# Performance work log

Measured on AMD Instinct MI355X. Metric: run time of the kernel, lower is better.

Reference implementation:

```python
import jax
import jax.numpy as jnp
import numpy as np

VOCAB = 16384
WIDTH = 256
BETA = 0.25
EPS = 1e-12  # F.normalize eps


def setup_inputs() -> dict:
    key = jax.random.key(0)
    k1, k2, k3 = jax.random.split(key, 3)
    class_tokens = jax.random.normal(k1, (32, 1, WIDTH), dtype=jnp.float32)
    patch_tokens = jax.random.normal(k2, (32, WIDTH, 16, 16), dtype=jnp.float32)
    W = jax.random.normal(k3, (VOCAB, WIDTH), dtype=jnp.float32) * 0.02  # codebook
    return {"class_tokens": class_tokens, "patch_tokens": patch_tokens, "W": W}


def _l2norm(x):
    return x / jnp.maximum(jnp.linalg.norm(x, axis=-1, keepdims=True), EPS)


def reference(class_tokens, patch_tokens, W):
    B, L, C = class_tokens.shape
    _, _, H, Wd = patch_tokens.shape
    # (B,C,H,W) -> (B,HW,C)
    pt = patch_tokens.reshape(B, C, H * Wd).transpose(0, 2, 1)
    NxC = jnp.concatenate([class_tokens, pt], axis=1).reshape(-1, C)  # [N,C]

    # vocab_norm branch: cosine-similarity argmax on detached, normalized vectors
    xn = _l2norm(jax.lax.stop_gradient(NxC))      # [N,C]
    Wn = _l2norm(W)                                # [V,C] (column-normalized W.T)
    sim = xn @ Wn.T                                # [N,V] big matmul
    idx = jnp.argmax(sim, axis=1)                  # [N]

    counts = jnp.zeros((VOCAB,), jnp.float32).at[idx].add(1.0)  # bincount

    fhat_g = W[idx]                                # codebook gather [N,C]
    vq_loss = BETA * jnp.mean((jax.lax.stop_gradient(fhat_g) - NxC) ** 2) \
              + jnp.mean((fhat_g - jax.lax.stop_gradient(NxC)) ** 2)

    # straight-through estimator
    fhat = jax.lax.stop_gradient(fhat_g - NxC) + NxC

    prob = counts / counts.sum()
    vocab_usage = jnp.mean((prob > 0.01 / VOCAB).astype(jnp.float32)) * 100.0

    fhat = fhat.reshape(B, L + H * Wd, C)
    fhat_class = fhat[:, :L, :]
    fhat_patch = fhat[:, L:, :].reshape(B, H, Wd, C).transpose(0, 3, 1, 2)
    return fhat_class, fhat_patch, vq_loss, vocab_usage
```

## Files before the change

kernel.cpp:

```cpp
#include <hip/hip_runtime.h>
#include <stdint.h>

#define VOCAB 16384
#define NB 32
#define NTOK 8224
#define MTILES 65
#define MP 8320
#define NBY 128
#define TILE_BYTES 65536
#define PHASE_BYTES 16384
#define NLOSS 2056
#define MWIN 2.25e-3f
#define TOKCHUNKS 520

typedef _Float16 half8 __attribute__((ext_vector_type(8)));
typedef float f4 __attribute__((ext_vector_type(4)));
typedef __attribute__((address_space(1))) const uint32_t* gas_t;
typedef __attribute__((address_space(3))) uint32_t* las_t;

__device__ __forceinline__ void async16(const void* g, void* l) {
    __builtin_amdgcn_global_load_lds((gas_t)g, (las_t)l, 16, 0, 0);
}

__device__ __forceinline__ unsigned long long key64(float v, int idx) {
    unsigned u = __float_as_uint(v);
    u = (u & 0x80000000u) ? ~u : (u | 0x80000000u);
    return ((unsigned long long)u << 32) | (unsigned)(~idx);
}

__device__ __forceinline__ float keyval(unsigned long long k) {
    unsigned u = (unsigned)(k >> 32);
    u = (u & 0x80000000u) ? (u & 0x7fffffffu) : ~u;
    return __uint_as_float(u);
}

__device__ __forceinline__ void merge2(unsigned long long& k1, unsigned long long& k2,
                                       unsigned long long p1, unsigned long long p2) {
    unsigned long long lo = k1 < p1 ? k1 : p1;
    k1 = k1 > p1 ? k1 : p1;
    unsigned long long m2 = k2 > p2 ? k2 : p2;
    k2 = lo > m2 ? lo : m2;
}

__global__ __launch_bounds__(256) void k_patch(const float* __restrict__ patch, float* __restrict__ tok) {
    __shared__ float t[64][65];
    int c0 = blockIdx.x * 64, p0 = blockIdx.y * 64, b = blockIdx.z;
    int tid = threadIdx.x;
    int l = tid & 63, w = tid >> 6;
    const float* src = patch + b * 65536;
#pragma unroll
    for (int i = 0; i < 16; ++i) {
        int row = i * 4 + w;
        t[row][l] = src[(c0 + row) * 256 + p0 + l];
    }
    __syncthreads();
#pragma unroll
    for (int i = 0; i < 16; ++i) {
        int prow = i * 4 + w;
        tok[(b * 257 + 1 + p0 + prow) * 256 + c0 + l] = t[l][prow];
    }
}

__global__ __launch_bounds__(256) void k_pack2(const float* __restrict__ tok, const float* __restrict__ cls,
                                               const float* __restrict__ W, char* __restrict__ apk,
                                               char* __restrict__ bpk, float* __restrict__ ntokv,
                                               float* __restrict__ nwv) {
    __shared__ float t[16][264];
    __shared__ float pr[16][16];
    __shared__ float sn[16];
    int g0 = blockIdx.x;
    bool isTok = g0 < TOKCHUNKS;
    int g = isTok ? g0 : g0 - TOKCHUNKS;
    char* dst = isTok ? apk : bpk;
    float* norms = isTok ? ntokv : nwv;
    int nrows = isTok ? NTOK : VOCAB;
    int row0 = g * 16;
    int tid = threadIdx.x;
    int rr = tid >> 4, cb = tid & 15;
    int grow = row0 + rr;
    const float* sp;
    if (isTok) {
        int b = grow / 257, s = grow - b * 257;
        sp = (s == 0) ? (cls + (size_t)b * 256 + cb * 16) : (tok + (size_t)grow * 256 + cb * 16);
    } else {
        sp = W + (size_t)grow * 256 + cb * 16;
    }
    float psum = 0.0f;
#pragma unroll
    for (int i = 0; i < 4; ++i) {
        float4 v = (grow < nrows) ? *(const float4*)(sp + i * 4) : make_float4(0.f, 0.f, 0.f, 0.f);
        *(float4*)&t[rr][cb * 16 + i * 4] = v;
        psum += v.x * v.x + v.y * v.y + v.z * v.z + v.w * v.w;
    }
    pr[rr][cb] = psum;
    __syncthreads();
    if (tid < 16) {
        float s = 0.0f;
#pragma unroll
        for (int j = 0; j < 16; ++j) s += pr[tid][j];
        float nv = fmaxf(sqrtf(s), 1e-12f);
        sn[tid] = nv;
        norms[row0 + tid] = nv;
    }
    __syncthreads();
    int c = tid & 63, pair = tid >> 6;
    int m = c & 15, jb = (c >> 4) * 8;
    float inv = 1.0f / sn[m];
    char* base = dst + (size_t)(g >> 3) * TILE_BYTES + (size_t)(g & 7) * 1024 + c * 16;
#pragma unroll
    for (int it = 0; it < 2; ++it) {
        int k32 = it * 4 + pair;
        const float* rowp = &t[m][k32 * 32 + jb];
        half8 o;
#pragma unroll
        for (int j = 0; j < 8; ++j) o[j] = (_Float16)(rowp[j] * inv);
        *(half8*)(base + (size_t)k32 * 8192) = o;
    }
}

__global__ __launch_bounds__(256) void k_sim(const char* __restrict__ apk, const char* __restrict__ bpk,
                                             unsigned long long* __restrict__ pb) {
    __shared__ char lds[32768];
    int id = blockIdx.x;
    int xcd = id & 7, r = id >> 3;
    int st = r / 104, within = r % 104;
    int stid = xcd * 10 + st;
    int sx = stid % 5, sy = stid / 5;
    int bx = sx * 13 + within % 13;
    int by = sy * 8 + within / 13;

    int tid = threadIdx.x;
    int ln = tid & 63, wv = tid >> 6;
    int mh = wv >> 1, nh = wv & 1;
    const char* abase = apk + (size_t)bx * TILE_BYTES;
    const char* bbase = bpk + (size_t)by * TILE_BYTES;

    f4 acc[4][4];
#pragma unroll
    for (int i = 0; i < 4; ++i)
#pragma unroll
        for (int j = 0; j < 4; ++j) acc[i][j] = (f4){0.f, 0.f, 0.f, 0.f};

#pragma unroll
    for (int i = 0; i < 8; ++i) {
        int c = wv * 8 + i;
        const char* g = (c < 16 ? abase + (c << 10) : bbase + ((c - 16) << 10)) + (ln << 4);
        async16(g, lds + (c << 10));
    }

    for (int p = 0; p < 4; ++p) {
        __syncthreads();
        half8 ah[2][4], bh[2][4];
#pragma unroll
        for (int s = 0; s < 2; ++s) {
            const half8* Af = (const half8*)(lds + s * 8192);
            const half8* Bf = (const half8*)(lds + 16384 + s * 8192);
#pragma unroll
            for (int mi = 0; mi < 4; ++mi) ah[s][mi] = Af[(mh * 4 + mi) * 64 + ln];
#pragma unroll
            for (int ni = 0; ni < 4; ++ni) bh[s][ni] = Bf[(nh * 4 + ni) * 64 + ln];
        }
        __syncthreads();
        if (p < 3) {
            const char* a2 = abase + (p + 1) * PHASE_BYTES;
            const char* b2 = bbase + (p + 1) * PHASE_BYTES;
#pragma unroll
            for (int i = 0; i < 8; ++i) {
                int c = wv * 8 + i;
                const char* g = (c < 16 ? a2 + (c << 10) : b2 + ((c - 16) << 10)) + (ln << 4);
                async16(g, lds + (c << 10));
            }
        }
#pragma unroll
        for (int s = 0; s < 2; ++s)
#pragma unroll
            for (int mi = 0; mi < 4; ++mi)
#pragma unroll
                for (int ni = 0; ni < 4; ++ni)
                    acc[mi][ni] = __builtin_amdgcn_mfma_f32_16x16x32_f16(bh[s][ni], ah[s][mi], acc[mi][ni], 0, 0, 0);
    }

    int col = ln & 15, quad = ln >> 4;
    unsigned long long* s1 = (unsigned long long*)lds;
    unsigned long long* s2 = (unsigned long long*)(lds + 2048);
    __syncthreads();
    int nbase = by * 128 + nh * 64 + quad * 4;
#pragma unroll
    for (int mi = 0; mi < 4; ++mi) {
        float v1 = -3.0f, v2 = -3.5f;
#pragma unroll
        for (int ni = 0; ni < 4; ++ni)
#pragma unroll
            for (int rg = 0; rg < 4; ++rg) {
                unsigned e = 15u - (unsigned)(ni * 4 + rg);
                float pv = __uint_as_float((__float_as_uint(acc[mi][ni][rg]) & 0xFFFFFFF0u) | e);
                float tmn = fminf(v1, pv);
                v1 = fmaxf(v1, pv);
                v2 = fmaxf(v2, tmn);
            }
        int o1 = 15 - (int)(__float_as_uint(v1) & 15u);
        int o2 = 15 - (int)(__float_as_uint(v2) & 15u);
        int n1 = ((o1 >> 2) << 4) | (o1 & 3);
        int n2 = ((o2 >> 2) << 4) | (o2 & 3);
        unsigned long long k1 = key64(v1, nbase + n1);
        unsigned long long k2 = key64(v2, nbase + n2);
#pragma unroll
        for (int off = 16; off < 64; off <<= 1) {
            unsigned long long p1 = __shfl_xor(k1, off);
            unsigned long long p2 = __shfl_xor(k2, off);
            merge2(k1, k2, p1, p2);
        }
        if (quad == 0) {
            int row = mh * 64 + mi * 16 + col;
            s1[row * 2 + nh] = k1;
            s2[row * 2 + nh] = k2;
        }
    }
    __syncthreads();
    if (tid < 128) {
        unsigned long long k1 = s1[tid * 2], k2 = s2[tid * 2];
        merge2(k1, k2, s1[tid * 2 + 1], s2[tid * 2 + 1]);
        ulonglong2 v; v.x = k1; v.y = k2;
        ((ulonglong2*)pb)[((size_t)bx * 128 + tid) * 128 + by] = v;
    }
}

__global__ __launch_bounds__(256) void k_gather(const unsigned long long* __restrict__ pb,
                                                const float* __restrict__ W, const float* __restrict__ tok,
                                                const float* __restrict__ cls,
                                                const float* __restrict__ ntok, const float* __restrict__ nw,
                                                float* __restrict__ out, int* __restrict__ idxbuf,
                                                float* __restrict__ lossbuf, unsigned int* __restrict__ used) {
    __shared__ float lp[4];
    int tid = threadIdx.x;
    int t = blockIdx.x * 4 + (tid >> 6);
    int ln = tid & 63, w = tid >> 6;
    const ulonglong2* pv = (const ulonglong2*)pb;
    ulonglong2 ea = pv[(size_t)t * 128 + ln];
    ulonglong2 eb = pv[(size_t)t * 128 + 64 + ln];
    unsigned long long g = ea.x > eb.x ? ea.x : eb.x;
#pragma unroll
    for (int off = 1; off < 64; off <<= 1) {
        unsigned long long o = __shfl_xor(g, off);
        if (o > g) g = o;
    }
    float T = keyval(g) - MWIN;
    int tq = t / 257, ts = t - tq * 257;
    const float* xrow = (ts == 0) ? (cls + (size_t)tq * 256) : (tok + (size_t)t * 256);
    f4 xv = *(const f4*)&xrow[ln * 4];
    float nt = ntok[t];
    unsigned long long k4[4] = {ea.x, ea.y, eb.x, eb.y};
    float bestv = -3.0f;
    int besti = 0x7fffffff;
#pragma unroll
    for (int gi = 0; gi < 4; ++gi) {
        unsigned long long mask = __ballot(keyval(k4[gi]) >= T);
        while (mask) {
            int src = __ffsll((unsigned long long)mask) - 1;
            mask &= mask - 1;
            unsigned long long ck = __shfl(k4[gi], src);
            int ci = (int)(~(unsigned)(ck & 0xffffffffu));
            f4 wc = *(const f4*)&W[(size_t)ci * 256 + ln * 4];
            float d = xv.x * wc.x + xv.y * wc.y + xv.z * wc.z + xv.w * wc.w;
#pragma unroll
            for (int off = 1; off < 64; off <<= 1) d += __shfl_xor(d, off);
            float sim = d / (nt * nw[ci]);
            if (sim > bestv || (sim == bestv && ci < besti)) { bestv = sim; besti = ci; }
        }
    }
    int bi = besti;
    f4 wr = *(const f4*)&W[(size_t)bi * 256 + ln * 4];
    float dx = wr.x - xv.x, dy = wr.y - xv.y, dz = wr.z - xv.z, dw = wr.w - xv.w;
    float ls = dx * dx + dy * dy + dz * dz + dw * dw;
#pragma unroll
    for (int off = 1; off < 64; off <<= 1) ls += __shfl_xor(ls, off);
    if (ln == 0) {
        lp[w] = ls;
        atomicOr(&used[bi >> 5], 1u << (bi & 31));
        idxbuf[t] = bi;
    }
    if (ts == 0) {
        *(f4*)&out[tq * 256 + ln * 4] = wr;
    }
    __syncthreads();
    if (tid == 0) lossbuf[blockIdx.x] = lp[0] + lp[1] + lp[2] + lp[3];
}

__global__ __launch_bounds__(256) void k_scatter(const int* __restrict__ idxbuf, const float* __restrict__ W,
                                                 float* __restrict__ out, const unsigned int* __restrict__ used,
                                                 const float* __restrict__ lossbuf) {
    __shared__ float t64[64][65];
    __shared__ int sidx[64];
    int c0 = blockIdx.x * 64, p0 = blockIdx.y * 64, b = blockIdx.z;
    int tid = threadIdx.x;
    if (tid < 64) sidx[tid] = idxbuf[b * 257 + 1 + p0 + tid];
    __syncthreads();
    int l = tid & 63, w = tid >> 6;
#pragma unroll
    for (int i = 0; i < 16; ++i) {
        int p = i * 4 + w;
        t64[p][l] = W[(size_t)sidx[p] * 256 + c0 + l];
    }
    __syncthreads();
#pragma unroll
    for (int i = 0; i < 16; ++i) {
        int c = i * 4 + w;
        out[8192 + (size_t)b * 65536 + (size_t)(c0 + c) * 256 + p0 + l] = t64[l][c];
    }
    if (blockIdx.x == 0 && blockIdx.y == 0 && blockIdx.z == 0) {
        int cnt = 0;
        float ls = 0.0f;
        for (int i = tid; i < VOCAB / 32; i += 256) cnt += __popc(used[i]);
        for (int i = tid; i < NLOSS; i += 256) ls += lossbuf[i];
#pragma unroll
        for (int off = 32; off > 0; off >>= 1) {
            cnt += __shfl_down(cnt, off);
            ls += __shfl_down(ls, off);
        }
        __shared__ int p4f[4];
        __shared__ float f4s[4];
        if ((tid & 63) == 0) { p4f[tid >> 6] = cnt; f4s[tid >> 6] = ls; }
        __syncthreads();
        if (tid == 0) {
            int c = p4f[0] + p4f[1] + p4f[2] + p4f[3];
            float lsum = f4s[0] + f4s[1] + f4s[2] + f4s[3];
            out[8192 + 2097152] = 1.25f * lsum / (float)(NTOK * 256);
            out[8192 + 2097152 + 1] = 100.0f * (float)c / (float)VOCAB;
        }
    }
}

extern "C" void kernel_launch(void* const* d_in, const int* in_sizes, int n_in,
                              void* d_out, int out_size, void* d_ws, size_t ws_size,
                              hipStream_t stream) {
    (void)in_sizes; (void)n_in; (void)out_size; (void)ws_size;
    const float* cls = (const float*)d_in[0];
    const float* patch = (const float*)d_in[1];
    const float* W = (const float*)d_in[2];
    float* out = (float*)d_out;

    char* ws = (char*)d_ws;
    float* tok = (float*)ws;
    char* apk = ws + (size_t)NTOK * 256 * 4;
    char* bpk = apk + (size_t)MTILES * TILE_BYTES;
    unsigned long long* pb = (unsigned long long*)(bpk + (size_t)NBY * TILE_BYTES);
    float* ntokv = (float*)(pb + (size_t)MP * NBY * 2);
    float* nwv = ntokv + MP;
    float* lossbuf = nwv + VOCAB;
    int* idxbuf = (int*)(lossbuf + NLOSS);
    unsigned int* used = (unsigned int*)(idxbuf + NTOK);

    hipMemsetAsync(used, 0, (VOCAB / 32) * sizeof(unsigned int), stream);

    k_patch<<<dim3(4, 4, NB), 256, 0, stream>>>(patch, tok);
    k_pack2<<<TOKCHUNKS + VOCAB / 16, 256, 0, stream>>>(tok, cls, W, apk, bpk, ntokv, nwv);
    k_sim<<<MTILES * NBY, 256, 0, stream>>>(apk, bpk, pb);
    k_gather<<<NLOSS, 256, 0, stream>>>(pb, W, tok, cls, ntokv, nwv, out, idxbuf, lossbuf, used);
    k_scatter<<<dim3(4, 4, NB), 256, 0, stream>>>(idxbuf, W, out, used, lossbuf);
}
```

Before: 203.2 us.

## Double-buffer LDS in similarity GEMM with explicit waitcnt prefetch pipeline

The similarity GEMM kernel's LDS doubles to two 32KB slots, and two K-phases are prefetched ahead. Explicit vmcnt/lgkmcnt waits and raw barriers replace __syncthreads, so global-to-LDS loads overlap MFMA work, and MFMA blocks run at raised wave priority. The top-2 update now uses a single fmed3 instruction instead of fmin plus fmax. The larger LDS footprint may reduce occupancy, and the hand-written waitcnt counts must match the number of outstanding async loads.

```diff
diff --git a/kernel.cpp b/kernel.cpp
--- a/kernel.cpp
+++ b/kernel.cpp
@@ -120,7 +120,7 @@
 
 __global__ __launch_bounds__(256) void k_sim(const char* __restrict__ apk, const char* __restrict__ bpk,
                                              unsigned long long* __restrict__ pb) {
-    __shared__ char lds[32768];
+    __shared__ char lds[65536];
     int id = blockIdx.x;
     int xcd = id & 7, r = id >> 3;
     int st = r / 104, within = r % 104;
@@ -141,49 +141,79 @@
 #pragma unroll
         for (int j = 0; j < 4; ++j) acc[i][j] = (f4){0.f, 0.f, 0.f, 0.f};
 
-#pragma unroll
-    for (int i = 0; i < 8; ++i) {
-        int c = wv * 8 + i;
-        const char* g = (c < 16 ? abase + (c << 10) : bbase + ((c - 16) << 10)) + (ln << 4);
-        async16(g, lds + (c << 10));
-    }
-
-    for (int p = 0; p < 4; ++p) {
-        __syncthreads();
-        half8 ah[2][4], bh[2][4];
-#pragma unroll
-        for (int s = 0; s < 2; ++s) {
-            const half8* Af = (const half8*)(lds + s * 8192);
-            const half8* Bf = (const half8*)(lds + 16384 + s * 8192);
-#pragma unroll
-            for (int mi = 0; mi < 4; ++mi) ah[s][mi] = Af[(mh * 4 + mi) * 64 + ln];
-#pragma unroll
-            for (int ni = 0; ni < 4; ++ni) bh[s][ni] = Bf[(nh * 4 + ni) * 64 + ln];
-        }
-        __syncthreads();
-        if (p < 3) {
-            const char* a2 = abase + (p + 1) * PHASE_BYTES;
-            const char* b2 = bbase + (p + 1) * PHASE_BYTES;
-#pragma unroll
-            for (int i = 0; i < 8; ++i) {
-                int c = wv * 8 + i;
-                const char* g = (c < 16 ? a2 + (c << 10) : b2 + ((c - 16) << 10)) + (ln << 4);
-                async16(g, lds + (c << 10));
-            }
-        }
-#pragma unroll
-        for (int s = 0; s < 2; ++s)
-#pragma unroll
-            for (int mi = 0; mi < 4; ++mi)
-#pragma unroll
-                for (int ni = 0; ni < 4; ++ni)
-                    acc[mi][ni] = __builtin_amdgcn_mfma_f32_16x16x32_f16(bh[s][ni], ah[s][mi], acc[mi][ni], 0, 0, 0);
+    auto STAGE = [&](int p, int slot) {
+#pragma unroll
+        for (int i = 0; i < 8; ++i) {
+            int c = wv * 8 + i;
+            const char* g = (c < 16 ? abase + p * PHASE_BYTES + (c << 10)
+                                    : bbase + p * PHASE_BYTES + ((c - 16) << 10)) + (ln << 4);
+            async16(g, lds + slot * 32768 + (c << 10));
+        }
+    };
+
+#define FRAGS(SB)                                                                     \
+    half8 ah[2][4], bh[2][4];                                                         \
+    {                                                                                 \
+        const char* sb_ = (SB);                                                       \
+        _Pragma("unroll")                                                             \
+        for (int s = 0; s < 2; ++s) {                                                 \
+            const half8* Af = (const half8*)(sb_ + s * 8192);                         \
+            const half8* Bf = (const half8*)(sb_ + 16384 + s * 8192);                 \
+            _Pragma("unroll")                                                         \
+            for (int mi = 0; mi < 4; ++mi) ah[s][mi] = Af[(mh * 4 + mi) * 64 + ln];   \
+            _Pragma("unroll")                                                         \
+            for (int ni = 0; ni < 4; ++ni) bh[s][ni] = Bf[(nh * 4 + ni) * 64 + ln];   \
+        }                                                                             \
+    }
+
+#define DOMFMA                                                                        \
+    __builtin_amdgcn_s_setprio(1);                                                    \
+    _Pragma("unroll")                                                                 \
+    for (int s = 0; s < 2; ++s)                                                       \
+        _Pragma("unroll")                                                             \
+        for (int mi = 0; mi < 4; ++mi)                                                \
+            _Pragma("unroll")                                                         \
+            for (int ni = 0; ni < 4; ++ni)                                            \
+                acc[mi][ni] = __builtin_amdgcn_mfma_f32_16x16x32_f16(bh[s][ni], ah[s][mi], acc[mi][ni], 0, 0, 0); \
+    __builtin_amdgcn_s_setprio(0);
+
+    STAGE(0, 0);
+    STAGE(1, 1);
+
+    {
+        asm volatile("s_waitcnt vmcnt(8)" ::: "memory");
+        __builtin_amdgcn_s_barrier();
+        FRAGS(lds);
+        asm volatile("s_waitcnt lgkmcnt(0)" ::: "memory");
+        __builtin_amdgcn_s_barrier();
+        STAGE(2, 0);
+        DOMFMA;
+    }
+    {
+        asm volatile("s_waitcnt vmcnt(8)" ::: "memory");
+        __builtin_amdgcn_s_barrier();
+        FRAGS(lds + 32768);
+        asm volatile("s_waitcnt lgkmcnt(0)" ::: "memory");
+        __builtin_amdgcn_s_barrier();
+        STAGE(3, 1);
+        DOMFMA;
+    }
+    {
+        asm volatile("s_waitcnt vmcnt(8)" ::: "memory");
+        __builtin_amdgcn_s_barrier();
+        FRAGS(lds);
+        DOMFMA;
+    }
+    {
+        asm volatile("s_waitcnt vmcnt(0)" ::: "memory");
+        __builtin_amdgcn_s_barrier();
+        FRAGS(lds + 32768);
+        DOMFMA;
     }
 
     int col = ln & 15, quad = ln >> 4;
     unsigned long long* s1 = (unsigned long long*)lds;
     unsigned long long* s2 = (unsigned long long*)(lds + 2048);
-    __syncthreads();
     int nbase = by * 128 + nh * 64 + quad * 4;
 #pragma unroll
     for (int mi = 0; mi < 4; ++mi) {
@@ -194,9 +224,8 @@
             for (int rg = 0; rg < 4; ++rg) {
                 unsigned e = 15u - (unsigned)(ni * 4 + rg);
                 float pv = __uint_as_float((__float_as_uint(acc[mi][ni][rg]) & 0xFFFFFFF0u) | e);
-                float tmn = fminf(v1, pv);
+                v2 = __builtin_amdgcn_fmed3f(v1, v2, pv);
                 v1 = fmaxf(v1, pv);
-                v2 = fmaxf(v2, tmn);
             }
         int o1 = 15 - (int)(__float_as_uint(v1) & 15u);
         int o2 = 15 - (int)(__float_as_uint(v2) & 15u);
@@ -223,6 +252,8 @@
         ulonglong2 v; v.x = k1; v.y = k2;
         ((ulonglong2*)pb)[((size_t)bx * 128 + tid) * 128 + by] = v;
     }
+#undef FRAGS
+#undef DOMFMA
 }
 
 __global__ __launch_bounds__(256) void k_gather(const unsigned long long* __restrict__ pb,
```

Measured after the change: 194.7 us. 4.2% less time.

## Stage full A tile in LDS, stream B fragments from registers, cheaper top-2 epilogue

Applied to the files above, without the earlier changes.

The sim kernel now loads the whole 64KB A tile into LDS in one shot and reads B fragments straight from global memory into double-buffered registers. This removes the per-phase LDS round-trip and its barriers for B. MFMA blocks are wrapped in setprio and sched_barrier to overlap global loads with compute. The top-2 epilogue packs the quad index into spare mantissa bits, uses fmed3 for the second maximum and shuffles 32-bit floats instead of 64-bit keys. In exchange, doubling LDS to 64KB lowers occupancy and further reduces mantissa precision for the similarity comparisons.

```diff
diff --git a/kernel.cpp b/kernel.cpp
--- a/kernel.cpp
+++ b/kernel.cpp
@@ -120,7 +120,7 @@
 
 __global__ __launch_bounds__(256) void k_sim(const char* __restrict__ apk, const char* __restrict__ bpk,
                                              unsigned long long* __restrict__ pb) {
-    __shared__ char lds[32768];
+    __shared__ char lds[65536];
     int id = blockIdx.x;
     int xcd = id & 7, r = id >> 3;
     int st = r / 104, within = r % 104;
@@ -133,7 +133,7 @@
     int ln = tid & 63, wv = tid >> 6;
     int mh = wv >> 1, nh = wv & 1;
     const char* abase = apk + (size_t)bx * TILE_BYTES;
-    const char* bbase = bpk + (size_t)by * TILE_BYTES;
+    const half8* Bg = (const half8*)(bpk + (size_t)by * TILE_BYTES);
 
     f4 acc[4][4];
 #pragma unroll
@@ -141,50 +141,58 @@
 #pragma unroll
         for (int j = 0; j < 4; ++j) acc[i][j] = (f4){0.f, 0.f, 0.f, 0.f};
 
-#pragma unroll
-    for (int i = 0; i < 8; ++i) {
-        int c = wv * 8 + i;
-        const char* g = (c < 16 ? abase + (c << 10) : bbase + ((c - 16) << 10)) + (ln << 4);
-        async16(g, lds + (c << 10));
-    }
-
-    for (int p = 0; p < 4; ++p) {
-        __syncthreads();
-        half8 ah[2][4], bh[2][4];
-#pragma unroll
-        for (int s = 0; s < 2; ++s) {
-            const half8* Af = (const half8*)(lds + s * 8192);
-            const half8* Bf = (const half8*)(lds + 16384 + s * 8192);
-#pragma unroll
-            for (int mi = 0; mi < 4; ++mi) ah[s][mi] = Af[(mh * 4 + mi) * 64 + ln];
-#pragma unroll
-            for (int ni = 0; ni < 4; ++ni) bh[s][ni] = Bf[(nh * 4 + ni) * 64 + ln];
-        }
-        __syncthreads();
-        if (p < 3) {
-            const char* a2 = abase + (p + 1) * PHASE_BYTES;
-            const char* b2 = bbase + (p + 1) * PHASE_BYTES;
-#pragma unroll
-            for (int i = 0; i < 8; ++i) {
-                int c = wv * 8 + i;
-                const char* g = (c < 16 ? a2 + (c << 10) : b2 + ((c - 16) << 10)) + (ln << 4);
-                async16(g, lds + (c << 10));
-            }
-        }
-#pragma unroll
-        for (int s = 0; s < 2; ++s)
-#pragma unroll
-            for (int mi = 0; mi < 4; ++mi)
-#pragma unroll
-                for (int ni = 0; ni < 4; ++ni)
-                    acc[mi][ni] = __builtin_amdgcn_mfma_f32_16x16x32_f16(bh[s][ni], ah[s][mi], acc[mi][ni], 0, 0, 0);
-    }
-
-    int col = ln & 15, quad = ln >> 4;
+    half8 b0[2][4], b1[2][4];
+#define LOADB(DST, P)                                                                 \
+    _Pragma("unroll")                                                                 \
+    for (int s = 0; s < 2; ++s)                                                       \
+        _Pragma("unroll")                                                             \
+        for (int ni = 0; ni < 4; ++ni)                                                \
+            DST[s][ni] = Bg[((P) * 16 + s * 8 + nh * 4 + ni) * 64 + ln];
+
+#define FRAGS(P)                                                                      \
+    half8 ah[2][4];                                                                   \
+    _Pragma("unroll")                                                                 \
+    for (int s = 0; s < 2; ++s) {                                                     \
+        const half8* Af = (const half8*)(lds + (P) * 16384 + s * 8192);               \
+        _Pragma("unroll")                                                             \
+        for (int mi = 0; mi < 4; ++mi) ah[s][mi] = Af[(mh * 4 + mi) * 64 + ln];       \
+    }
+
+#define DOMFMA(BH)                                                                    \
+    __builtin_amdgcn_s_setprio(1);                                                    \
+    _Pragma("unroll")                                                                 \
+    for (int s = 0; s < 2; ++s)                                                       \
+        _Pragma("unroll")                                                             \
+        for (int mi = 0; mi < 4; ++mi)                                                \
+            _Pragma("unroll")                                                         \
+            for (int ni = 0; ni < 4; ++ni)                                            \
+                acc[mi][ni] = __builtin_amdgcn_mfma_f32_16x16x32_f16(BH[s][ni], ah[s][mi], acc[mi][ni], 0, 0, 0); \
+    __builtin_amdgcn_s_setprio(0);
+
+    LOADB(b0, 0);
+#pragma unroll
+    for (int i = 0; i < 16; ++i) {
+        int c = wv * 16 + i;
+        async16(abase + (c << 10) + (ln << 4), lds + (c << 10));
+    }
+    LOADB(b1, 1);
+    __syncthreads();
+
+    { FRAGS(0); DOMFMA(b0); }
+    __builtin_amdgcn_sched_barrier(0);
+    { LOADB(b0, 2); FRAGS(1); DOMFMA(b1); }
+    __builtin_amdgcn_sched_barrier(0);
+    { LOADB(b1, 3); FRAGS(2); DOMFMA(b0); }
+    __builtin_amdgcn_sched_barrier(0);
+    { FRAGS(3); DOMFMA(b1); }
+
+    __syncthreads();
     unsigned long long* s1 = (unsigned long long*)lds;
     unsigned long long* s2 = (unsigned long long*)(lds + 2048);
-    __syncthreads();
-    int nbase = by * 128 + nh * 64 + quad * 4;
+
+    int col = ln & 15, quad = ln >> 4;
+    unsigned qb = (unsigned)(3 - quad) << 4;
+    int nbase0 = by * 128 + nh * 64;
 #pragma unroll
     for (int mi = 0; mi < 4; ++mi) {
         float v1 = -3.0f, v2 = -3.5f;
@@ -194,26 +202,29 @@
             for (int rg = 0; rg < 4; ++rg) {
                 unsigned e = 15u - (unsigned)(ni * 4 + rg);
                 float pv = __uint_as_float((__float_as_uint(acc[mi][ni][rg]) & 0xFFFFFFF0u) | e);
-                float tmn = fminf(v1, pv);
+                v2 = __builtin_amdgcn_fmed3f(v1, v2, pv);
                 v1 = fmaxf(v1, pv);
-                v2 = fmaxf(v2, tmn);
             }
-        int o1 = 15 - (int)(__float_as_uint(v1) & 15u);
-        int o2 = 15 - (int)(__float_as_uint(v2) & 15u);
-        int n1 = ((o1 >> 2) << 4) | (o1 & 3);
-        int n2 = ((o2 >> 2) << 4) | (o2 & 3);
-        unsigned long long k1 = key64(v1, nbase + n1);
-        unsigned long long k2 = key64(v2, nbase + n2);
+        float w1 = __uint_as_float((__float_as_uint(v1) & 0xFFFFFFCFu) | qb);
+        float w2 = __uint_as_float((__float_as_uint(v2) & 0xFFFFFFCFu) | qb);
+        v1 = fmaxf(w1, w2);
+        v2 = fminf(w1, w2);
 #pragma unroll
         for (int off = 16; off < 64; off <<= 1) {
-            unsigned long long p1 = __shfl_xor(k1, off);
-            unsigned long long p2 = __shfl_xor(k2, off);
-            merge2(k1, k2, p1, p2);
+            float p1 = __shfl_xor(v1, off);
+            float p2 = __shfl_xor(v2, off);
+            v2 = __builtin_amdgcn_fmed3f(v1, p1, fmaxf(v2, p2));
+            v1 = fmaxf(v1, p1);
         }
         if (quad == 0) {
+            unsigned u1 = __float_as_uint(v1), u2 = __float_as_uint(v2);
+            int q1 = 3 - (int)((u1 >> 4) & 3u), o1 = 15 - (int)(u1 & 15u);
+            int q2 = 3 - (int)((u2 >> 4) & 3u), o2 = 15 - (int)(u2 & 15u);
+            int n1 = ((o1 >> 2) << 4) + q1 * 4 + (o1 & 3);
+            int n2 = ((o2 >> 2) << 4) + q2 * 4 + (o2 & 3);
             int row = mh * 64 + mi * 16 + col;
-            s1[row * 2 + nh] = k1;
-            s2[row * 2 + nh] = k2;
+            s1[row * 2 + nh] = key64(v1, nbase0 + n1);
+            s2[row * 2 + nh] = key64(v2, nbase0 + n2);
         }
     }
     __syncthreads();
@@ -223,6 +234,9 @@
         ulonglong2 v; v.x = k1; v.y = k2;
         ((ulonglong2*)pb)[((size_t)bx * 128 + tid) * 128 + by] = v;
     }
+#undef LOADB
+#undef FRAGS
+#undef DOMFMA
 }
 
 __global__ __launch_bounds__(256) void k_gather(const unsigned long long* __restrict__ pb,
```

New measurement: 192.9 us. -5.1%, faster.
